# Optimization experiments

Hardware: AMD Instinct MI355X
Metric: run time of the kernel (lower is better)

## Reference

```python
import jax, jax.numpy as jnp
import numpy as np

B, K, S, E = 16, 16, 512, 512   # batch, k_history, max_spikes_in_batch, embed_dim
L, H, KVH, D = 16, 8, 2, 64     # num_latents, heads, kv heads, head_dim
BIN = 50                        # bin_size (RoPE table length)


def setup_inputs() -> dict:
    key = jax.random.key(0)
    ks = jax.random.split(key, 8)
    spike = jax.random.normal(ks[0], (B, K, S, E), dtype=jnp.float32)
    offsets = jax.random.randint(ks[1], (B, K, S), 0, BIN)
    spike_lengths = jax.random.randint(ks[2], (B, K), 1, S + 1)  # >=1 so no fully-masked row
    # standard RoPE tables of shape (BIN, D)
    inv_freq = 1.0 / (10000.0 ** (np.arange(0, D, 2, dtype=np.float32) / D))
    freqs = np.outer(np.arange(BIN, dtype=np.float32), inv_freq)      # (BIN, D/2)
    emb = np.concatenate([freqs, freqs], axis=-1)                     # (BIN, D)
    cos = jnp.asarray(np.cos(emb), dtype=jnp.float32)
    sin = jnp.asarray(np.sin(emb), dtype=jnp.float32)
    latent_query = jax.random.normal(ks[3], (L, E), dtype=jnp.float32)
    Wq = jax.random.normal(ks[4], (H * D, E), dtype=jnp.float32) * (E ** -0.5)
    Wk = jax.random.normal(ks[5], (KVH * D, E), dtype=jnp.float32) * (E ** -0.5)
    Wv = jax.random.normal(ks[6], (KVH * D, E), dtype=jnp.float32) * (E ** -0.5)
    Wo = jax.random.normal(ks[7], (E, H * D), dtype=jnp.float32) * ((H * D) ** -0.5)
    return dict(spike=spike, offsets=offsets, spike_lengths=spike_lengths,
                cos=cos, sin=sin, latent_query=latent_query,
                Wq=Wq, Wk=Wk, Wv=Wv, Wo=Wo)


def rotate_half(x):
    h = x.shape[-1] // 2
    return jnp.concatenate([-x[..., h:], x[..., :h]], axis=-1)


def reference(spike, offsets, spike_lengths, cos, sin, latent_query, Wq, Wk, Wv, Wo):
    n_rep = H // KVH
    # fixed learnable queries, shared across batch / k_history
    xq = (latent_query @ Wq.T).reshape(L, H, D)                         # (L,H,D)
    xk = jnp.einsum('bkse,he->bksh', spike, Wk).reshape(B, K, S, KVH, D)
    xv = jnp.einsum('bkse,he->bksh', spike, Wv).reshape(B, K, S, KVH, D)
    # inline RoPE on keys only (is_decoder=False), driven by per-token offsets
    cos_sel = cos[offsets][..., None, :]                                # (B,K,S,1,D)
    sin_sel = sin[offsets][..., None, :]
    xk = xk * cos_sel + rotate_half(xk) * sin_sel
    # repeat_kv: interleaved head repetition (matches torch expand+reshape)
    xk = jnp.repeat(xk, n_rep, axis=3)                                  # (B,K,S,H,D)
    xv = jnp.repeat(xv, n_rep, axis=3)
    scores = jnp.einsum('lhd,bkshd->bkhls', xq, xk) / jnp.sqrt(jnp.float32(D))
    # ragged-length mask: positions >= spike_lengths are invalid
    pos = jnp.arange(S)
    mask = pos[None, None, None, None, :] >= spike_lengths[:, :, None, None, None]
    scores = jnp.where(mask, -jnp.inf, scores)
    attn = jax.nn.softmax(scores, axis=-1)                              # (B,K,H,L,S)
    out = jnp.einsum('bkhls,bkshd->bklhd', attn, xv).reshape(B, K, L, H * D)
    return out @ Wo.T                                                   # (B,K,L,E)
```

## Files before the change

kernel.cpp:

```cpp
#include <hip/hip_runtime.h>
#include <hip/hip_bf16.h>
#include <stdint.h>

typedef __attribute__((ext_vector_type(8))) short bf16x8;
typedef __attribute__((ext_vector_type(4))) float f32x4;

union FragU { uint4 u; bf16x8 v; };

#define Bn 16
#define Kn 16
#define Sn 512
#define En 512
#define Ln 16
#define Hn 8
#define Dn 64
#define BKTOT 256
#define MTOT (BKTOT*Sn)

__device__ __forceinline__ uint32_t pack_bf16(float lo, float hi) {
  uint32_t a = __float_as_uint(lo) + 0x8000u;
  uint32_t b = __float_as_uint(hi) + 0x8000u;
  return __builtin_amdgcn_perm(b, a, 0x07060302u);
}
__device__ __forceinline__ uint16_t bf16_1(float x) {
  __hip_bfloat16 h = __float2bfloat16(x);
  return *(uint16_t*)&h;
}

__global__ __launch_bounds__(256)
void xq_kernel(const float* __restrict__ latent, const float* __restrict__ Wq,
               float* __restrict__ xq)
{
  const int j = blockIdx.x;
  const int t = threadIdx.x;
  const float w0 = Wq[j*En + t];
  const float w1 = Wq[j*En + t + 256];
  float part[Ln];
#pragma unroll
  for (int l = 0; l < Ln; ++l)
    part[l] = w0 * latent[l*En + t] + w1 * latent[l*En + t + 256];
#pragma unroll
  for (int l = 0; l < Ln; ++l) {
    float v = part[l];
#pragma unroll
    for (int off = 32; off > 0; off >>= 1) v += __shfl_down(v, off, 64);
    part[l] = v;
  }
  __shared__ float red[4][Ln];
  const int lane = t & 63, wv = t >> 6;
  if (lane == 0) {
#pragma unroll
    for (int l = 0; l < Ln; ++l) red[wv][l] = part[l];
  }
  __syncthreads();
  if (t < Ln)
    xq[t*En + j] = red[0][t] + red[1][t] + red[2][t] + red[3][t];
}

__global__ __launch_bounds__(256)
void kvproj_kernel(const float* __restrict__ spike, const int* __restrict__ offsets,
                   const float* __restrict__ cosT, const float* __restrict__ sinT,
                   const float* __restrict__ Wk, const float* __restrict__ Wv,
                   uint16_t* __restrict__ Kbuf, uint16_t* __restrict__ Vt)
{
  __shared__ __align__(16) uint32_t As[64*20];
  __shared__ __align__(16) uint32_t Bs[256*20];
  const int t = threadIdx.x;
  const int m0 = blockIdx.x * 64;
  const int lane = t & 63, wv = t >> 6;
  const int quad = lane >> 4, lr = lane & 15;

  f32x4 acc[4][4];
#pragma unroll
  for (int i=0;i<4;i++)
#pragma unroll
    for (int j=0;j<4;j++) acc[i][j] = (f32x4){0.f,0.f,0.f,0.f};

  const int srow = t >> 3;
  const int scg  = t & 7;

  for (int k0 = 0; k0 < En; k0 += 32) {
#pragma unroll
    for (int i = 0; i < 2; ++i) {
      const int row = srow + 32*i;
      float4 v = *(const float4*)&spike[(size_t)(m0 + row)*En + k0 + scg*4];
      uint2 p; p.x = pack_bf16(v.x, v.y); p.y = pack_bf16(v.z, v.w);
      *(uint2*)&As[row*20 + scg*2] = p;
    }
#pragma unroll
    for (int i = 0; i < 8; ++i) {
      const int row = srow + 32*i;
      const float* src = (i < 4) ? &Wk[(size_t)row*En] : &Wv[(size_t)(row-128)*En];
      float4 v = *(const float4*)&src[k0 + scg*4];
      uint2 p; p.x = pack_bf16(v.x, v.y); p.y = pack_bf16(v.z, v.w);
      *(uint2*)&Bs[row*20 + scg*2] = p;
    }
    __syncthreads();
    FragU aF[4], bF[4];
#pragma unroll
    for (int mi=0;mi<4;mi++) aF[mi].u = *(const uint4*)&As[(mi*16+lr)*20 + quad*4];
#pragma unroll
    for (int ni=0;ni<4;ni++) bF[ni].u = *(const uint4*)&Bs[(wv*64 + ni*16 + lr)*20 + quad*4];
#pragma unroll
    for (int mi=0;mi<4;mi++)
#pragma unroll
      for (int ni=0;ni<4;ni++)
        acc[mi][ni] = __builtin_amdgcn_mfma_f32_16x16x32_bf16(aF[mi].v, bF[ni].v, acc[mi][ni], 0,0,0);
    __syncthreads();
  }

  const int bk = m0 >> 9;
  const int sbase = m0 & 511;
  if (wv < 2) {
#pragma unroll
    for (int mi=0;mi<4;mi++) {
#pragma unroll
      for (int r=0;r<4;r++) {
        const int s = sbase + mi*16 + quad*4 + r;
        const int off = offsets[m0 + mi*16 + quad*4 + r];
#pragma unroll
        for (int ni=0;ni<4;ni++) {
          const int d = ni*16 + lr;
          const float v = acc[mi][ni][r];
          const float p = acc[mi][ni^2][r];
          const float rot = (ni < 2) ? -p : p;
          const float c  = cosT[off*Dn + d];
          const float sn = sinT[off*Dn + d];
          Kbuf[((size_t)(bk*512 + s))*128 + wv*64 + d] = bf16_1(v*c + rot*sn);
        }
      }
    }
  } else {
    const int nbase = (wv - 2) * 64;
#pragma unroll
    for (int mi=0;mi<4;mi++) {
#pragma unroll
      for (int ni=0;ni<4;ni++) {
        const int np = nbase + ni*16 + lr;
        const int s  = sbase + mi*16 + quad*4;
        uint2 pk;
        pk.x = pack_bf16(acc[mi][ni][0], acc[mi][ni][1]);
        pk.y = pack_bf16(acc[mi][ni][2], acc[mi][ni][3]);
        *(uint2*)&Vt[((size_t)(bk*128 + np))*512 + s] = pk;
      }
    }
  }
}

__global__ __launch_bounds__(256)
void attn_kernel(const float* __restrict__ xq, const uint16_t* __restrict__ Kbuf,
                 const uint16_t* __restrict__ Vt, const int* __restrict__ lengths,
                 float* __restrict__ attn_out)
{
  __shared__ __align__(16) uint16_t Ks [128*72];
  __shared__ __align__(16) uint16_t Vts[64*136];
  __shared__ __align__(16) uint16_t Ps [4*16*136];

  const int t = threadIdx.x;
  const int bk = blockIdx.x >> 1, kvh = blockIdx.x & 1;
  const int w = t >> 6, lane = t & 63;
  const int quad = lane >> 4, lr = lane & 15;
  const int h = kvh*4 + w;
  const int len = lengths[bk];

  FragU aQ[2];
#pragma unroll
  for (int kk=0;kk<2;kk++) {
    const float* qp = &xq[lr*En + h*Dn + kk*32 + quad*8];
    float4 q0 = *(const float4*)qp;
    float4 q1 = *(const float4*)(qp + 4);
    aQ[kk].u.x = pack_bf16(q0.x*0.125f, q0.y*0.125f);
    aQ[kk].u.y = pack_bf16(q0.z*0.125f, q0.w*0.125f);
    aQ[kk].u.z = pack_bf16(q1.x*0.125f, q1.y*0.125f);
    aQ[kk].u.w = pack_bf16(q1.z*0.125f, q1.w*0.125f);
  }

  float m_run[4], l_run[4], alpha[4];
  f32x4 oacc[4];
#pragma unroll
  for (int r=0;r<4;r++){ m_run[r] = -3.0e38f; l_run[r] = 0.f; }
#pragma unroll
  for (int nd=0;nd<4;nd++) oacc[nd] = (f32x4){0.f,0.f,0.f,0.f};

  const int krow = t >> 1, kseg = t & 1;
  const int vrow = t >> 2, vseg = t & 3;

  for (int c = 0; c < 4; ++c) {
    const int s0 = c * 128;
    if (s0 >= len) break;
    __syncthreads();
    {
      const uint16_t* g = &Kbuf[((size_t)(bk*512 + s0 + krow))*128 + kvh*64 + kseg*32];
      uint16_t* dst = &Ks[krow*72 + kseg*32];
      uint4 a0 = *(const uint4*)g, a1 = *(const uint4*)(g+8);
      uint4 a2 = *(const uint4*)(g+16), a3 = *(const uint4*)(g+24);
      *(uint4*)dst = a0; *(uint4*)(dst+8) = a1; *(uint4*)(dst+16) = a2; *(uint4*)(dst+24) = a3;

      const uint16_t* gv = &Vt[((size_t)(bk*128 + kvh*64 + vrow))*512 + s0 + vseg*32];
      uint16_t* dv = &Vts[vrow*136 + vseg*32];
      uint4 b0 = *(const uint4*)gv, b1 = *(const uint4*)(gv+8);
      uint4 b2 = *(const uint4*)(gv+16), b3 = *(const uint4*)(gv+24);
      *(uint4*)dv = b0; *(uint4*)(dv+8) = b1; *(uint4*)(dv+16) = b2; *(uint4*)(dv+24) = b3;
    }
    __syncthreads();

    f32x4 sc[8];
#pragma unroll
    for (int ni=0;ni<8;ni++) {
      FragU b0, b1;
      b0.u = *(const uint4*)&Ks[(ni*16+lr)*72 + quad*8];
      b1.u = *(const uint4*)&Ks[(ni*16+lr)*72 + 32 + quad*8];
      f32x4 a = (f32x4){0.f,0.f,0.f,0.f};
      a = __builtin_amdgcn_mfma_f32_16x16x32_bf16(aQ[0].v, b0.v, a, 0,0,0);
      a = __builtin_amdgcn_mfma_f32_16x16x32_bf16(aQ[1].v, b1.v, a, 0,0,0);
      sc[ni] = a;
    }
#pragma unroll
    for (int ni=0;ni<8;ni++)
      if (s0 + ni*16 + lr >= len)
        sc[ni] = (f32x4){-3.0e38f,-3.0e38f,-3.0e38f,-3.0e38f};

#pragma unroll
    for (int r=0;r<4;r++) {
      float mx = sc[0][r];
#pragma unroll
      for (int ni=1;ni<8;ni++) mx = fmaxf(mx, sc[ni][r]);
#pragma unroll
      for (int o=1;o<16;o<<=1) mx = fmaxf(mx, __shfl_xor(mx, o, 16));
      const float mnew = fmaxf(m_run[r], mx);
      alpha[r] = __expf(m_run[r] - mnew);
      m_run[r] = mnew;
      float ssum = 0.f;
#pragma unroll
      for (int ni=0;ni<8;ni++) {
        float p = __expf(sc[ni][r] - mnew);
        sc[ni][r] = p;
        ssum += p;
      }
#pragma unroll
      for (int o=1;o<16;o<<=1) ssum += __shfl_xor(ssum, o, 16);
      l_run[r] = l_run[r]*alpha[r] + ssum;
    }

#pragma unroll
    for (int ni=0;ni<8;ni++)
#pragma unroll
      for (int r=0;r<4;r++)
        Ps[(w*16 + quad*4 + r)*136 + ni*16 + lr] = bf16_1(sc[ni][r]);

#pragma unroll
    for (int nd=0;nd<4;nd++)
#pragma unroll
      for (int r=0;r<4;r++) oacc[nd][r] *= alpha[r];

#pragma unroll
    for (int kk=0;kk<4;kk++) {
      FragU aP;
      aP.u = *(const uint4*)&Ps[(w*16 + lr)*136 + kk*32 + quad*8];
#pragma unroll
      for (int nd=0;nd<4;nd++) {
        FragU bV;
        bV.u = *(const uint4*)&Vts[(nd*16+lr)*136 + kk*32 + quad*8];
        oacc[nd] = __builtin_amdgcn_mfma_f32_16x16x32_bf16(aP.v, bV.v, oacc[nd], 0,0,0);
      }
    }
  }

#pragma unroll
  for (int r=0;r<4;r++) {
    const float rs = 1.0f / l_run[r];
    const int l = quad*4 + r;
#pragma unroll
    for (int nd=0;nd<4;nd++)
      attn_out[((size_t)(bk*16 + l))*512 + h*64 + nd*16 + lr] = oacc[nd][r] * rs;
  }
}

__global__ __launch_bounds__(256)
void oproj_kernel(const float* __restrict__ A, const float* __restrict__ Wo,
                  float* __restrict__ out)
{
  __shared__ __align__(16) float As[64*36];
  __shared__ __align__(16) float Bs[64*36];
  const int t = threadIdx.x;
  const int r0 = (blockIdx.x >> 3) * 64;
  const int e0 = (blockIdx.x & 7) * 64;
  const int ty = t >> 4, tx = t & 15;
  float acc[4][4];
#pragma unroll
  for (int i=0;i<4;i++)
#pragma unroll
    for (int j=0;j<4;j++) acc[i][j] = 0.f;

  const int srow = t >> 3, scg = t & 7;
  for (int k0=0;k0<512;k0+=32) {
#pragma unroll
    for (int i=0;i<2;i++) {
      const int row = srow + 32*i;
      *(float4*)&As[row*36 + scg*4] = *(const float4*)&A [(size_t)(r0+row)*512 + k0 + scg*4];
      *(float4*)&Bs[row*36 + scg*4] = *(const float4*)&Wo[(size_t)(e0+row)*512 + k0 + scg*4];
    }
    __syncthreads();
#pragma unroll
    for (int kk=0;kk<32;kk+=4) {
      float4 av[4], bv[4];
#pragma unroll
      for (int i=0;i<4;i++) av[i] = *(const float4*)&As[(ty+16*i)*36 + kk];
#pragma unroll
      for (int j=0;j<4;j++) bv[j] = *(const float4*)&Bs[(tx+16*j)*36 + kk];
#pragma unroll
      for (int i=0;i<4;i++)
#pragma unroll
        for (int j=0;j<4;j++)
          acc[i][j] += av[i].x*bv[j].x + av[i].y*bv[j].y + av[i].z*bv[j].z + av[i].w*bv[j].w;
    }
    __syncthreads();
  }
#pragma unroll
  for (int i=0;i<4;i++)
#pragma unroll
    for (int j=0;j<4;j++)
      out[(size_t)(r0+ty+16*i)*512 + e0 + tx + 16*j] = acc[i][j];
}

extern "C" void kernel_launch(void* const* d_in, const int* in_sizes, int n_in,
                              void* d_out, int out_size, void* d_ws, size_t ws_size,
                              hipStream_t stream)
{
  const float* spike   = (const float*)d_in[0];
  const int*   offsets = (const int*)d_in[1];
  const int*   lengths = (const int*)d_in[2];
  const float* cosT    = (const float*)d_in[3];
  const float* sinT    = (const float*)d_in[4];
  const float* latent  = (const float*)d_in[5];
  const float* Wq      = (const float*)d_in[6];
  const float* Wk      = (const float*)d_in[7];
  const float* Wv      = (const float*)d_in[8];
  const float* Wo      = (const float*)d_in[9];
  float* out = (float*)d_out;

  char* ws = (char*)d_ws;
  float*    xq   = (float*)ws;
  uint16_t* Kbuf = (uint16_t*)(ws + 65536);
  uint16_t* Vt   = (uint16_t*)(ws + 65536 + (33554432ull));
  float* attn_out = (float*)(ws + 65536 + 67108864ull);

  hipLaunchKernelGGL(xq_kernel,     dim3(512),  dim3(256), 0, stream, latent, Wq, xq);
  hipLaunchKernelGGL(kvproj_kernel, dim3(2048), dim3(256), 0, stream, spike, offsets, cosT, sinT, Wk, Wv, Kbuf, Vt);
  hipLaunchKernelGGL(attn_kernel,   dim3(512),  dim3(256), 0, stream, xq, Kbuf, Vt, lengths, attn_out);
  hipLaunchKernelGGL(oproj_kernel,  dim3(512),  dim3(256), 0, stream, attn_out, Wo, out);
}
```

Measured before the change: 496.9 us.

## Pre-convert weights to swizzled bf16, use direct-to-LDS loads and MFMA output projection

Adds a kernel that converts Wk/Wv to a bf16 XOR-swizzled layout and Wo to bf16 once per call. The KV projection then streams weights with global_load_lds instead of reconverting fp32 weights in every block, and uses a 64-wide k step. The attention output is stored as bf16, and the output projection is rewritten from a scalar fp32 GEMM into a 128x128-tiled bf16 MFMA GEMM. This trades an extra launch and lower precision in the output projection for less redundant conversion and more compute throughput.

```diff
diff --git a/kernel.cpp b/kernel.cpp
--- a/kernel.cpp
+++ b/kernel.cpp
@@ -26,6 +26,11 @@
   __hip_bfloat16 h = __float2bfloat16(x);
   return *(uint16_t*)&h;
 }
+__device__ __forceinline__ void gload_lds16(const void* g, void* l) {
+  __builtin_amdgcn_global_load_lds(
+      (const __attribute__((address_space(1))) uint32_t*)g,
+      (__attribute__((address_space(3))) uint32_t*)l, 16, 0, 0);
+}
 
 __global__ __launch_bounds__(256)
 void xq_kernel(const float* __restrict__ latent, const float* __restrict__ Wq,
@@ -58,13 +63,45 @@
 }
 
 __global__ __launch_bounds__(256)
+void wconv_kernel(const float* __restrict__ Wk, const float* __restrict__ Wv,
+                  const float* __restrict__ Wo,
+                  uint4* __restrict__ Wsw, uint4* __restrict__ Wob)
+{
+  const int t = threadIdx.x;
+  const int b = blockIdx.x;
+  if (b < 64) {
+    const int idx = b*256 + t;
+    const int kb = idx >> 11;
+    const int rem = idx & 2047;
+    const int n = rem >> 3, p = rem & 7;
+    const int c = p ^ (n & 7);
+    const float* src = (n < 128 ? Wk + (size_t)n*En : Wv + (size_t)(n-128)*En) + kb*64 + c*8;
+    float4 v0 = *(const float4*)src;
+    float4 v1 = *(const float4*)(src+4);
+    uint4 o;
+    o.x = pack_bf16(v0.x,v0.y); o.y = pack_bf16(v0.z,v0.w);
+    o.z = pack_bf16(v1.x,v1.y); o.w = pack_bf16(v1.z,v1.w);
+    Wsw[idx] = o;
+  } else {
+    const int idx = (b-64)*256 + t;
+    const float* src = Wo + (size_t)idx*8;
+    float4 v0 = *(const float4*)src;
+    float4 v1 = *(const float4*)(src+4);
+    uint4 o;
+    o.x = pack_bf16(v0.x,v0.y); o.y = pack_bf16(v0.z,v0.w);
+    o.z = pack_bf16(v1.x,v1.y); o.w = pack_bf16(v1.z,v1.w);
+    Wob[idx] = o;
+  }
+}
+
+__global__ __launch_bounds__(256)
 void kvproj_kernel(const float* __restrict__ spike, const int* __restrict__ offsets,
                    const float* __restrict__ cosT, const float* __restrict__ sinT,
-                   const float* __restrict__ Wk, const float* __restrict__ Wv,
+                   const uint4* __restrict__ Wsw,
                    uint16_t* __restrict__ Kbuf, uint16_t* __restrict__ Vt)
 {
-  __shared__ __align__(16) uint32_t As[64*20];
-  __shared__ __align__(16) uint32_t Bs[256*20];
+  __shared__ __align__(16) uint16_t Bs[256*64];
+  __shared__ __align__(16) uint16_t As[64*72];
   const int t = threadIdx.x;
   const int m0 = blockIdx.x * 64;
   const int lane = t & 63, wv = t >> 6;
@@ -76,36 +113,44 @@
 #pragma unroll
     for (int j=0;j<4;j++) acc[i][j] = (f32x4){0.f,0.f,0.f,0.f};
 
-  const int srow = t >> 3;
-  const int scg  = t & 7;
-
-  for (int k0 = 0; k0 < En; k0 += 32) {
-#pragma unroll
-    for (int i = 0; i < 2; ++i) {
-      const int row = srow + 32*i;
-      float4 v = *(const float4*)&spike[(size_t)(m0 + row)*En + k0 + scg*4];
-      uint2 p; p.x = pack_bf16(v.x, v.y); p.y = pack_bf16(v.z, v.w);
-      *(uint2*)&As[row*20 + scg*2] = p;
-    }
-#pragma unroll
-    for (int i = 0; i < 8; ++i) {
-      const int row = srow + 32*i;
-      const float* src = (i < 4) ? &Wk[(size_t)row*En] : &Wv[(size_t)(row-128)*En];
-      float4 v = *(const float4*)&src[k0 + scg*4];
-      uint2 p; p.x = pack_bf16(v.x, v.y); p.y = pack_bf16(v.z, v.w);
-      *(uint2*)&Bs[row*20 + scg*2] = p;
-    }
-    __syncthreads();
-    FragU aF[4], bF[4];
-#pragma unroll
-    for (int mi=0;mi<4;mi++) aF[mi].u = *(const uint4*)&As[(mi*16+lr)*20 + quad*4];
-#pragma unroll
-    for (int ni=0;ni<4;ni++) bF[ni].u = *(const uint4*)&Bs[(wv*64 + ni*16 + lr)*20 + quad*4];
-#pragma unroll
-    for (int mi=0;mi<4;mi++)
-#pragma unroll
-      for (int ni=0;ni<4;ni++)
-        acc[mi][ni] = __builtin_amdgcn_mfma_f32_16x16x32_bf16(aF[mi].v, bF[ni].v, acc[mi][ni], 0,0,0);
+  const int arow = t >> 3;
+  const int aseg = t & 7;
+
+  for (int kb = 0; kb < 8; ++kb) {
+    const char* gb = (const char*)(Wsw + kb*2048) + (wv*64 + lane)*16;
+    char* lb = (char*)Bs + wv*1024;
+#pragma unroll
+    for (int i = 0; i < 8; ++i)
+      gload_lds16(gb + i*4096, lb + i*4096);
+#pragma unroll
+    for (int j = 0; j < 2; ++j) {
+      const int row = arow + 32*j;
+      const float* src = &spike[(size_t)(m0+row)*En + kb*64 + aseg*8];
+      float4 v0 = *(const float4*)src;
+      float4 v1 = *(const float4*)(src+4);
+      uint4 o;
+      o.x = pack_bf16(v0.x,v0.y); o.y = pack_bf16(v0.z,v0.w);
+      o.z = pack_bf16(v1.x,v1.y); o.w = pack_bf16(v1.z,v1.w);
+      *(uint4*)&As[row*72 + aseg*8] = o;
+    }
+    __syncthreads();
+#pragma unroll
+    for (int kk = 0; kk < 2; ++kk) {
+      const int c = kk*4 + quad;
+      FragU aF[4], bF[4];
+#pragma unroll
+      for (int mi=0;mi<4;mi++) aF[mi].u = *(const uint4*)&As[(mi*16+lr)*72 + c*8];
+#pragma unroll
+      for (int ni=0;ni<4;ni++) {
+        const int n = wv*64 + ni*16 + lr;
+        bF[ni].u = *(const uint4*)&Bs[n*64 + (c ^ (n&7))*8];
+      }
+#pragma unroll
+      for (int mi=0;mi<4;mi++)
+#pragma unroll
+        for (int ni=0;ni<4;ni++)
+          acc[mi][ni] = __builtin_amdgcn_mfma_f32_16x16x32_bf16(aF[mi].v, bF[ni].v, acc[mi][ni], 0,0,0);
+    }
     __syncthreads();
   }
 
@@ -124,9 +169,9 @@
           const float v = acc[mi][ni][r];
           const float p = acc[mi][ni^2][r];
           const float rot = (ni < 2) ? -p : p;
-          const float c  = cosT[off*Dn + d];
-          const float sn = sinT[off*Dn + d];
-          Kbuf[((size_t)(bk*512 + s))*128 + wv*64 + d] = bf16_1(v*c + rot*sn);
+          const float cc  = cosT[off*Dn + d];
+          const float sn  = sinT[off*Dn + d];
+          Kbuf[((size_t)(bk*512 + s))*128 + wv*64 + d] = bf16_1(v*cc + rot*sn);
         }
       }
     }
@@ -150,7 +195,7 @@
 __global__ __launch_bounds__(256)
 void attn_kernel(const float* __restrict__ xq, const uint16_t* __restrict__ Kbuf,
                  const uint16_t* __restrict__ Vt, const int* __restrict__ lengths,
-                 float* __restrict__ attn_out)
+                 uint16_t* __restrict__ attn_out)
 {
   __shared__ __align__(16) uint16_t Ks [128*72];
   __shared__ __align__(16) uint16_t Vts[64*136];
@@ -272,55 +317,61 @@
     const int l = quad*4 + r;
 #pragma unroll
     for (int nd=0;nd<4;nd++)
-      attn_out[((size_t)(bk*16 + l))*512 + h*64 + nd*16 + lr] = oacc[nd][r] * rs;
+      attn_out[((size_t)(bk*16 + l))*512 + h*64 + nd*16 + lr] = bf16_1(oacc[nd][r] * rs);
   }
 }
 
 __global__ __launch_bounds__(256)
-void oproj_kernel(const float* __restrict__ A, const float* __restrict__ Wo,
+void oproj_kernel(const uint16_t* __restrict__ Ab, const uint16_t* __restrict__ Wob,
                   float* __restrict__ out)
 {
-  __shared__ __align__(16) float As[64*36];
-  __shared__ __align__(16) float Bs[64*36];
+  __shared__ __align__(16) uint16_t As[128*72];
+  __shared__ __align__(16) uint16_t Bs[128*72];
   const int t = threadIdx.x;
-  const int r0 = (blockIdx.x >> 3) * 64;
-  const int e0 = (blockIdx.x & 7) * 64;
-  const int ty = t >> 4, tx = t & 15;
-  float acc[4][4];
+  const int m0 = (blockIdx.x >> 2) * 128;
+  const int n0 = (blockIdx.x & 3) * 128;
+  const int lane = t & 63, wv = t >> 6;
+  const int quad = lane >> 4, lr = lane & 15;
+  const int wm = wv >> 1, wn = wv & 1;
+
+  f32x4 acc[4][4];
 #pragma unroll
   for (int i=0;i<4;i++)
 #pragma unroll
-    for (int j=0;j<4;j++) acc[i][j] = 0.f;
-
-  const int srow = t >> 3, scg = t & 7;
-  for (int k0=0;k0<512;k0+=32) {
-#pragma unroll
-    for (int i=0;i<2;i++) {
-      const int row = srow + 32*i;
-      *(float4*)&As[row*36 + scg*4] = *(const float4*)&A [(size_t)(r0+row)*512 + k0 + scg*4];
-      *(float4*)&Bs[row*36 + scg*4] = *(const float4*)&Wo[(size_t)(e0+row)*512 + k0 + scg*4];
-    }
-    __syncthreads();
-#pragma unroll
-    for (int kk=0;kk<32;kk+=4) {
-      float4 av[4], bv[4];
-#pragma unroll
-      for (int i=0;i<4;i++) av[i] = *(const float4*)&As[(ty+16*i)*36 + kk];
-#pragma unroll
-      for (int j=0;j<4;j++) bv[j] = *(const float4*)&Bs[(tx+16*j)*36 + kk];
-#pragma unroll
-      for (int i=0;i<4;i++)
-#pragma unroll
-        for (int j=0;j<4;j++)
-          acc[i][j] += av[i].x*bv[j].x + av[i].y*bv[j].y + av[i].z*bv[j].z + av[i].w*bv[j].w;
-    }
-    __syncthreads();
-  }
-#pragma unroll
-  for (int i=0;i<4;i++)
-#pragma unroll
-    for (int j=0;j<4;j++)
-      out[(size_t)(r0+ty+16*i)*512 + e0 + tx + 16*j] = acc[i][j];
+    for (int j=0;j<4;j++) acc[i][j] = (f32x4){0.f,0.f,0.f,0.f};
+
+  const int srow = t >> 3, sseg = t & 7;
+  for (int kb = 0; kb < 8; ++kb) {
+#pragma unroll
+    for (int j = 0; j < 4; ++j) {
+      const int row = srow + 32*j;
+      *(uint4*)&As[row*72 + sseg*8] = *(const uint4*)&Ab [(size_t)(m0+row)*512 + kb*64 + sseg*8];
+      *(uint4*)&Bs[row*72 + sseg*8] = *(const uint4*)&Wob[(size_t)(n0+row)*512 + kb*64 + sseg*8];
+    }
+    __syncthreads();
+#pragma unroll
+    for (int kk = 0; kk < 2; ++kk) {
+      const int c = kk*4 + quad;
+      FragU aF[4], bF[4];
+#pragma unroll
+      for (int mi=0;mi<4;mi++) aF[mi].u = *(const uint4*)&As[(wm*64+mi*16+lr)*72 + c*8];
+#pragma unroll
+      for (int ni=0;ni<4;ni++) bF[ni].u = *(const uint4*)&Bs[(wn*64+ni*16+lr)*72 + c*8];
+#pragma unroll
+      for (int mi=0;mi<4;mi++)
+#pragma unroll
+        for (int ni=0;ni<4;ni++)
+          acc[mi][ni] = __builtin_amdgcn_mfma_f32_16x16x32_bf16(aF[mi].v, bF[ni].v, acc[mi][ni], 0,0,0);
+    }
+    __syncthreads();
+  }
+#pragma unroll
+  for (int mi=0;mi<4;mi++)
+#pragma unroll
+    for (int r=0;r<4;r++)
+#pragma unroll
+      for (int ni=0;ni<4;ni++)
+        out[(size_t)(m0 + wm*64 + mi*16 + quad*4 + r)*512 + n0 + wn*64 + ni*16 + lr] = acc[mi][ni][r];
 }
 
 extern "C" void kernel_launch(void* const* d_in, const int* in_sizes, int n_in,
@@ -341,12 +392,15 @@
 
   char* ws = (char*)d_ws;
   float*    xq   = (float*)ws;
-  uint16_t* Kbuf = (uint16_t*)(ws + 65536);
-  uint16_t* Vt   = (uint16_t*)(ws + 65536 + (33554432ull));
-  float* attn_out = (float*)(ws + 65536 + 67108864ull);
+  uint4*    Wsw  = (uint4*)(ws + 65536);
+  uint4*    Wob  = (uint4*)(ws + 65536 + 262144);
+  uint16_t* Kbuf = (uint16_t*)(ws + 1048576);
+  uint16_t* Vt   = (uint16_t*)(ws + 1048576 + 33554432ull);
+  uint16_t* attn_out = (uint16_t*)(ws + 1048576 + 67108864ull);
 
   hipLaunchKernelGGL(xq_kernel,     dim3(512),  dim3(256), 0, stream, latent, Wq, xq);
-  hipLaunchKernelGGL(kvproj_kernel, dim3(2048), dim3(256), 0, stream, spike, offsets, cosT, sinT, Wk, Wv, Kbuf, Vt);
+  hipLaunchKernelGGL(wconv_kernel,  dim3(192),  dim3(256), 0, stream, Wk, Wv, Wo, Wsw, Wob);
+  hipLaunchKernelGGL(kvproj_kernel, dim3(2048), dim3(256), 0, stream, spike, offsets, cosT, sinT, Wsw, Kbuf, Vt);
   hipLaunchKernelGGL(attn_kernel,   dim3(512),  dim3(256), 0, stream, xq, Kbuf, Vt, lengths, attn_out);
-  hipLaunchKernelGGL(oproj_kernel,  dim3(512),  dim3(256), 0, stream, attn_out, Wo, out);
-}
+  hipLaunchKernelGGL(oproj_kernel,  dim3(128),  dim3(256), 0, stream, attn_out, (const uint16_t*)Wob, out);
+}
```

New measurement: 436.4 us. 1.14x faster.
